# Kernel optimization log

Hardware: AMD Instinct MI355X
Metric: run time of the kernel (lower is better)

Reference implementation:

```python
import jax, jax.numpy as jnp
import numpy as np

N_NODES = 100000
M_EDGES = 500000
D = 128
L = 2
LRELU_SLOPE = 0.01
LN_EPS = 1e-5


def layer_norm(x, g, b):
    mu = jnp.mean(x, axis=-1, keepdims=True)
    var = jnp.var(x, axis=-1, keepdims=True)
    return (x - mu) * jax.lax.rsqrt(var + LN_EPS) * g + b


def leaky_relu(x):
    return jnp.where(x >= 0, x, LRELU_SLOPE * x)


def setup_inputs() -> dict:
    key = jax.random.key(0)
    ks = jax.random.split(key, 12)
    s = 1.0 / np.sqrt(D)
    inp = {
        "H": jax.random.normal(ks[0], (N_NODES, D), jnp.float32),
        "E": jax.random.normal(ks[1], (M_EDGES, D), jnp.float32),
        "ht": jax.random.randint(ks[2], (M_EDGES, 2), 0, N_NODES, jnp.int64) if jax.config.jax_enable_x64 else jax.random.randint(ks[2], (M_EDGES, 2), 0, N_NODES).astype(jnp.int32),
        "queries": jax.random.randint(ks[3], (M_EDGES,), 0, 2).astype(jnp.int32),
        # per-layer params stacked on leading L axis
        "W_eu": jax.random.uniform(ks[4], (L, 3 * D, D), jnp.float32, -s, s),
        "b_eu": jnp.zeros((L, D), jnp.float32),
        "ln_e_g": jnp.ones((L, D), jnp.float32),
        "ln_e_b": jnp.zeros((L, D), jnp.float32),
        "W_fwd": jax.random.uniform(ks[5], (L, 2 * D, D), jnp.float32, -s, s),
        "b_fwd": jnp.zeros((L, D), jnp.float32),
        "W_back": jax.random.uniform(ks[6], (L, 2 * D, D), jnp.float32, -s, s),
        "b_back": jnp.zeros((L, D), jnp.float32),
        "ln_h_g": jnp.ones((L, D), jnp.float32),
        "ln_h_b": jnp.zeros((L, D), jnp.float32),
    }
    return inp


def aggregate_messages(ht, messages_fwd, messages_back, n):
    # destinations: fwd msgs go to tails, back msgs go to heads
    msg_dst = jnp.concatenate([ht[:, 1], ht[:, 0]])  # [2m]
    messages = jnp.concatenate([messages_fwd, messages_back], axis=0)  # [2m, d]
    agg = jax.ops.segment_sum(messages, msg_dst, num_segments=n)  # [n, d]
    counts = jax.ops.segment_sum(jnp.ones_like(msg_dst, jnp.float32), msg_dst, num_segments=n)
    # torch yields nan/inf for count-0 nodes; clamp to 1 (0/1 = 0) for stability
    return agg / jnp.maximum(counts, 1.0)[:, None]


def reference(H, E, ht, queries, W_eu, b_eu, ln_e_g, ln_e_b,
              W_fwd, b_fwd, W_back, b_back, ln_h_g, ln_h_b):
    n = H.shape[0]
    for l in range(L):
        # --- EdgeUpdateLayer ---
        head_rep = H[ht[:, 0]]  # [m, d]
        tail_rep = H[ht[:, 1]]  # [m, d]
        triple = jnp.concatenate([head_rep, E, tail_rep], axis=1)  # [m, 3d]
        eu = leaky_relu(triple @ W_eu[l] + b_eu[l])
        E = layer_norm(eu + E, ln_e_g[l], ln_e_b[l])
        # --- MessagePassingLayer ---
        msgs_fwd = jnp.concatenate([H[ht[:, 0]], E], axis=1) @ W_fwd[l] + b_fwd[l]
        msgs_back = jnp.concatenate([H[ht[:, 1]], E], axis=1) @ W_back[l] + b_back[l]
        agg = aggregate_messages(ht, msgs_fwd, msgs_back, n)
        H = layer_norm(leaky_relu(agg) + H, ln_h_g[l], ln_h_b[l])
    return H
```

## Files before the change

kernel.cpp:

```cpp
#include <hip/hip_runtime.h>

#define N_NODES 100000
#define M_EDGES 500000
#define D 128
#define SLOPE 0.01f
#define EPS 1e-5f

typedef __attribute__((ext_vector_type(8))) short bf16x8;
typedef __attribute__((ext_vector_type(4))) float f32x4;
typedef __attribute__((ext_vector_type(4))) unsigned int u32x4;

__device__ __forceinline__ unsigned short f2bf(float f) {
    union { float f; unsigned u; } v; v.f = f;
    unsigned r = v.u + 0x7FFF + ((v.u >> 16) & 1);
    return (unsigned short)(r >> 16);
}
__device__ __forceinline__ float bf2f(unsigned short u) {
    union { unsigned u; float f; } v; v.u = ((unsigned)u) << 16; return v.f;
}
__device__ __forceinline__ u32x4 pack8v(f32x4 a, f32x4 b) {
    u32x4 r;
    r.x = ((unsigned)f2bf(a.y) << 16) | f2bf(a.x);
    r.y = ((unsigned)f2bf(a.w) << 16) | f2bf(a.z);
    r.z = ((unsigned)f2bf(b.y) << 16) | f2bf(b.x);
    r.w = ((unsigned)f2bf(b.w) << 16) | f2bf(b.z);
    return r;
}

__global__ void wconv_kernel(const float* __restrict__ src, unsigned short* __restrict__ dst,
                             int K, int total)
{
    int i = blockIdx.x * 256 + threadIdx.x;
    if (i >= total) return;
    int layer_sz = K * 128;
    int l = i / layer_sz;
    int r = i - l * layer_sz;
    int j    = r & 7;
    int lane = (r >> 3) & 63;
    int nt   = (r >> 9) & 7;
    int kk   = r >> 12;
    int row  = kk * 32 + ((lane >> 4) << 3) + j;
    int col  = nt * 16 + (lane & 15);
    dst[i] = f2bf(src[(size_t)l * layer_sz + row * 128 + col]);
}

__global__ void h2b_kernel(const float* __restrict__ src, unsigned short* __restrict__ dst, int total8)
{
    int i = blockIdx.x * 256 + threadIdx.x;
    if (i >= total8) return;
    f32x4 a = ((const f32x4*)src)[2 * i];
    f32x4 b = ((const f32x4*)src)[2 * i + 1];
    ((u32x4*)dst)[i] = pack8v(a, b);
}

__global__ void count_kernel(const int* __restrict__ ht, int* __restrict__ cnt, int m)
{
    int e = blockIdx.x * 256 + threadIdx.x;
    if (e < m) {
        atomicAdd(&cnt[ht[2 * e]],     1);
        atomicAdd(&cnt[ht[2 * e + 1]], 1);
    }
}

__global__ void scanA_kernel(const int* __restrict__ cnt, int* __restrict__ partial,
                             int* __restrict__ bsum, int n)
{
    __shared__ int tmp[256];
    int t = threadIdx.x, i = blockIdx.x * 256 + t;
    int v = (i < n) ? cnt[i] : 0;
    tmp[t] = v;
    __syncthreads();
    for (int s = 1; s < 256; s <<= 1) {
        int x = (t >= s) ? tmp[t - s] : 0;
        __syncthreads();
        tmp[t] += x;
        __syncthreads();
    }
    if (i < n) partial[i] = tmp[t] - v;
    if (t == 255) bsum[blockIdx.x] = tmp[255];
}

__global__ void scanB_kernel(int* __restrict__ bsum, int nb)
{
    __shared__ int tmp[512];
    int t = threadIdx.x;
    int v = (t < nb) ? bsum[t] : 0;
    tmp[t] = v;
    __syncthreads();
    for (int s = 1; s < 512; s <<= 1) {
        int x = (t >= s) ? tmp[t - s] : 0;
        __syncthreads();
        tmp[t] += x;
        __syncthreads();
    }
    if (t < nb) bsum[t] = tmp[t] - v;
}

__global__ void scanC_kernel(const int* __restrict__ partial, const int* __restrict__ bsum,
                             int* __restrict__ off, int* __restrict__ pos, int n)
{
    int i = blockIdx.x * 256 + threadIdx.x;
    if (i < n) {
        int o = partial[i] + bsum[blockIdx.x];
        off[i] = o;
        pos[i] = o;
    }
    if (i == 0) off[n] = 2 * M_EDGES;
}

__global__ void fill_kernel(const int* __restrict__ ht, int* __restrict__ pos,
                            int* __restrict__ slotF, int* __restrict__ slotB, int m)
{
    int e = blockIdx.x * 256 + threadIdx.x;
    if (e < m) {
        int2 p = ((const int2*)ht)[e];
        slotF[e] = atomicAdd(&pos[p.y], 1);
        slotB[e] = atomicAdd(&pos[p.x], 1);
    }
}

template <bool E_F32, bool WRITE_E>
__global__ __launch_bounds__(64, 2)
void edge_mfma_kernel(const unsigned short* __restrict__ Hb,
                      const float* __restrict__ E0,
                      const unsigned short* __restrict__ Ebf,
                      unsigned short* __restrict__ Eout,
                      const int* __restrict__ ht,
                      const unsigned short* __restrict__ Weu,
                      const unsigned short* __restrict__ Wf,
                      const unsigned short* __restrict__ Wb,
                      const float* __restrict__ beu,
                      const float* __restrict__ lneg, const float* __restrict__ lneb,
                      const float* __restrict__ bfw, const float* __restrict__ bbw,
                      const int* __restrict__ slotF, const int* __restrict__ slotB,
                      unsigned short* __restrict__ msg)
{
    __shared__ unsigned char en[16384];

    const int ln  = threadIdx.x;
    const int g   = ln >> 4;
    const int c15 = ln & 15;
    const int ew0 = blockIdx.x * 64;

    int eL = ew0 + ln; if (eL >= M_EDGES) eL = M_EDGES - 1;
    const int slotFv = slotF[eL];
    const int slotBv = slotB[eL];

#pragma unroll
    for (int it = 0; it < 16; ++it) {
        int lin = it * 1024 + ln * 16;
        int row = lin >> 8;
        int e   = ew0 + row;
        int es  = (e < M_EDGES) ? e : (M_EDGES - 1);
        int elem = (lin & 255) >> 1;
        u32x4 pk;
        if (E_F32) {
            const float* s = E0 + (size_t)es * D + elem;
            pk = pack8v(*(const f32x4*)s, *(const f32x4*)(s + 4));
        } else {
            pk = *(const u32x4*)(Ebf + (size_t)es * D + elem);
        }
        *(u32x4*)(en + (lin ^ ((row & 7) << 4))) = pk;
    }

    const unsigned short* hrow[4];
    const unsigned short* trow[4];
#pragma unroll
    for (int m = 0; m < 4; ++m) {
        int e = ew0 + m * 16 + c15;
        int es = (e < M_EDGES) ? e : (M_EDGES - 1);
        int2 p = ((const int2*)ht)[es];
        hrow[m] = Hb + (size_t)p.x * D;
        trow[m] = Hb + (size_t)p.y * D;
    }
    const int swz = (c15 & 7) << 4;

    f32x4 acc[4][8];

#pragma unroll
    for (int m = 0; m < 4; ++m)
#pragma unroll
        for (int nt = 0; nt < 8; ++nt) acc[m][nt] = (f32x4){0.f, 0.f, 0.f, 0.f};

    {
        const u32x4* Wg = (const u32x4*)Weu;
        u32x4 bc[8];
        bf16x8 a[4], an[4];
        auto loadA = [&](int kk, int m) -> bf16x8 {
            if (kk < 4)
                return *(const bf16x8*)(hrow[m] + kk * 32 + g * 8);
            if (kk < 8)
                return *(const bf16x8*)(en + (((m * 16 + c15) * 256 + (kk - 4) * 64 + g * 16) ^ swz));
            return *(const bf16x8*)(trow[m] + (kk - 8) * 32 + g * 8);
        };
#pragma unroll
        for (int nt = 0; nt < 8; ++nt) bc[nt] = Wg[nt * 64 + ln];
#pragma unroll
        for (int m = 0; m < 4; ++m) a[m] = loadA(0, m);
#pragma unroll
        for (int kk = 0; kk < 12; ++kk) {
            if (kk < 11) {
#pragma unroll
                for (int m = 0; m < 4; ++m) an[m] = loadA(kk + 1, m);
            }
#pragma unroll
            for (int nt = 0; nt < 8; ++nt) {
                bf16x8 b = *(const bf16x8*)&bc[nt];
#pragma unroll
                for (int m = 0; m < 4; ++m)
                    acc[m][nt] = __builtin_amdgcn_mfma_f32_16x16x32_bf16(a[m], b, acc[m][nt], 0, 0, 0);
                if (kk < 11) bc[nt] = Wg[(kk + 1) * 512 + nt * 64 + ln];
            }
#pragma unroll
            for (int m = 0; m < 4; ++m) a[m] = an[m];
        }
    }

    {
        float be[8], lg[8], lb[8];
#pragma unroll
        for (int nt = 0; nt < 8; ++nt) {
            be[nt] = beu[nt * 16 + c15];
            lg[nt] = lneg[nt * 16 + c15];
            lb[nt] = lneb[nt * 16 + c15];
        }
#pragma unroll
        for (int m = 0; m < 4; ++m) {
            float s[4] = {0.f,0.f,0.f,0.f}, ss[4] = {0.f,0.f,0.f,0.f};
#pragma unroll
            for (int nt = 0; nt < 8; ++nt) {
#pragma unroll
                for (int r = 0; r < 4; ++r) {
                    int row = m * 16 + g * 4 + r;
                    float x = acc[m][nt][r] + be[nt];
                    x = (x >= 0.f) ? x : SLOPE * x;
                    int lin = row * 256 + (nt * 16 + c15) * 2;
                    x += bf2f(*(const unsigned short*)(en + (lin ^ ((row & 7) << 4))));
                    acc[m][nt][r] = x;
                    s[r] += x; ss[r] += x * x;
                }
            }
#pragma unroll
            for (int d = 1; d < 16; d <<= 1) {
#pragma unroll
                for (int r = 0; r < 4; ++r) {
                    s[r]  += __shfl_xor(s[r],  d);
                    ss[r] += __shfl_xor(ss[r], d);
                }
            }
            float mu[4], rs[4];
#pragma unroll
            for (int r = 0; r < 4; ++r) {
                mu[r] = s[r] * (1.0f / 128.0f);
                float var = ss[r] * (1.0f / 128.0f) - mu[r] * mu[r];
                rs[r] = rsqrtf(var + EPS);
            }
#pragma unroll
            for (int nt = 0; nt < 8; ++nt) {
#pragma unroll
                for (int r = 0; r < 4; ++r) {
                    int row = m * 16 + g * 4 + r;
                    float xn = (acc[m][nt][r] - mu[r]) * rs[r] * lg[nt] + lb[nt];
                    int lin = row * 256 + (nt * 16 + c15) * 2;
                    *(unsigned short*)(en + (lin ^ ((row & 7) << 4))) = f2bf(xn);
                }
            }
        }
    }

    if (WRITE_E) {
#pragma unroll
        for (int it = 0; it < 16; ++it) {
            int lin = it * 1024 + ln * 16;
            int row = lin >> 8;
            int e   = ew0 + row;
            if (e < M_EDGES)
                *(u32x4*)(Eout + (size_t)e * D + ((lin & 255) >> 1)) =
                    *(const u32x4*)(en + (lin ^ ((row & 7) << 4)));
        }
    }

#pragma unroll
    for (int pass = 0; pass < 2; ++pass) {
        const u32x4* Wg = (const u32x4*)(pass == 0 ? Wf : Wb);
#pragma unroll
        for (int m = 0; m < 4; ++m)
#pragma unroll
            for (int nt = 0; nt < 8; ++nt) acc[m][nt] = (f32x4){0.f, 0.f, 0.f, 0.f};

        {
            u32x4 bc[8];
            bf16x8 a[4], an[4];
            auto loadA = [&](int kk, int m) -> bf16x8 {
                if (kk < 4)
                    return *(const bf16x8*)((pass == 0 ? hrow[m] : trow[m]) + kk * 32 + g * 8);
                return *(const bf16x8*)(en + (((m * 16 + c15) * 256 + (kk - 4) * 64 + g * 16) ^ swz));
            };
#pragma unroll
            for (int nt = 0; nt < 8; ++nt) bc[nt] = Wg[nt * 64 + ln];
#pragma unroll
            for (int m = 0; m < 4; ++m) a[m] = loadA(0, m);
#pragma unroll
            for (int kk = 0; kk < 8; ++kk) {
                if (kk < 7) {
#pragma unroll
                    for (int m = 0; m < 4; ++m) an[m] = loadA(kk + 1, m);
                }
#pragma unroll
                for (int nt = 0; nt < 8; ++nt) {
                    bf16x8 b = *(const bf16x8*)&bc[nt];
#pragma unroll
                    for (int m = 0; m < 4; ++m)
                        acc[m][nt] = __builtin_amdgcn_mfma_f32_16x16x32_bf16(a[m], b, acc[m][nt], 0, 0, 0);
                    if (kk < 7) bc[nt] = Wg[(kk + 1) * 512 + nt * 64 + ln];
                }
#pragma unroll
                for (int m = 0; m < 4; ++m) a[m] = an[m];
            }
        }

        {
            const float* bias = pass == 0 ? bfw : bbw;
            const int slotv = pass == 0 ? slotFv : slotBv;
            float bv[8];
#pragma unroll
            for (int nt = 0; nt < 8; ++nt) bv[nt] = bias[nt * 16 + c15];
#pragma unroll
            for (int m = 0; m < 4; ++m) {
#pragma unroll
                for (int r = 0; r < 4; ++r) {
                    int erow = m * 16 + g * 4 + r;
                    bool val = (ew0 + erow < M_EDGES);
                    int slot = __shfl(slotv, erow);
                    unsigned* base = (unsigned*)(msg + (size_t)slot * D + (c15 & ~1));
#pragma unroll
                    for (int nt = 0; nt < 8; ++nt) {
                        float v = acc[m][nt][r] + bv[nt];
                        float o = __shfl_xor(v, 1);
                        float lo = (ln & 1) ? o : v;
                        float hi = (ln & 1) ? v : o;
                        unsigned pk = ((unsigned)f2bf(hi) << 16) | f2bf(lo);
                        if (val && ((ln & 1) == (nt >> 2)))
                            base[nt * 8] = pk;
                    }
                }
            }
        }
    }
}

__global__ __launch_bounds__(256)
void node_kernel(const float* __restrict__ Hin, const unsigned short* __restrict__ msg,
                 const int* __restrict__ off, const float* __restrict__ g,
                 const float* __restrict__ b, float* __restrict__ Hout,
                 unsigned short* __restrict__ Hb, int n)
{
    const int wave = threadIdx.x >> 6, lane = threadIdx.x & 63;
    const int node = blockIdx.x * 4 + wave;
    if (node >= n) return;

    const int beg = off[node], end = off[node + 1];
    const float inv = 1.0f / fmaxf((float)(end - beg), 1.0f);
    const unsigned* mb = (const unsigned*)msg;

    float a0 = 0.f, a1 = 0.f;
    int i = beg;
    for (; i + 1 < end; i += 2) {
        unsigned v0 = mb[(size_t)i * 64 + lane];
        unsigned v1 = mb[(size_t)(i + 1) * 64 + lane];
        a0 += bf2f((unsigned short)(v0 & 0xffff)) + bf2f((unsigned short)(v1 & 0xffff));
        a1 += bf2f((unsigned short)(v0 >> 16))    + bf2f((unsigned short)(v1 >> 16));
    }
    if (i < end) {
        unsigned v0 = mb[(size_t)i * 64 + lane];
        a0 += bf2f((unsigned short)(v0 & 0xffff));
        a1 += bf2f((unsigned short)(v0 >> 16));
    }

    a0 *= inv; a1 *= inv;
    a0 = (a0 >= 0.f) ? a0 : SLOPE * a0;
    a1 = (a1 >= 0.f) ? a1 : SLOPE * a1;

    size_t base = (size_t)node * D + 2 * lane;
    float x0 = a0 + Hin[base];
    float x1 = a1 + Hin[base + 1];

    float s = x0 + x1, ss = x0 * x0 + x1 * x1;
#pragma unroll
    for (int d = 1; d < 64; d <<= 1) {
        s  += __shfl_xor(s, d);
        ss += __shfl_xor(ss, d);
    }
    float mu  = s * (1.0f / 128.0f);
    float var = ss * (1.0f / 128.0f) - mu * mu;
    float rs  = rsqrtf(var + EPS);

    float o0 = (x0 - mu) * rs * g[2 * lane]     + b[2 * lane];
    float o1 = (x1 - mu) * rs * g[2 * lane + 1] + b[2 * lane + 1];
    Hout[base]     = o0;
    Hout[base + 1] = o1;
    Hb[base]       = f2bf(o0);
    Hb[base + 1]   = f2bf(o1);
}

extern "C" void kernel_launch(void* const* d_in, const int* in_sizes, int n_in,
                              void* d_out, int out_size, void* d_ws, size_t ws_size,
                              hipStream_t stream)
{
    const float* H0   = (const float*)d_in[0];
    const float* E0   = (const float*)d_in[1];
    const int*   ht   = (const int*)d_in[2];
    const float* Weu  = (const float*)d_in[4];
    const float* beu  = (const float*)d_in[5];
    const float* lneg = (const float*)d_in[6];
    const float* lneb = (const float*)d_in[7];
    const float* Wf   = (const float*)d_in[8];
    const float* bfw  = (const float*)d_in[9];
    const float* Wb   = (const float*)d_in[10];
    const float* bbw  = (const float*)d_in[11];
    const float* lnhg = (const float*)d_in[12];
    const float* lnhb = (const float*)d_in[13];

    float* Hout = (float*)d_out;

    char* ws = (char*)d_ws;
    unsigned short* msg    = (unsigned short*)(ws);
    unsigned short* Ebuf   = (unsigned short*)(ws + 256000000);
    unsigned short* Hb     = (unsigned short*)(ws + 384000000);
    unsigned short* Weu_sw = (unsigned short*)(ws + 409600000);
    unsigned short* Wf_sw  = (unsigned short*)(ws + 409796608);
    unsigned short* Wb_sw  = (unsigned short*)(ws + 409927680);
    int*            cnt    = (int*)(ws + 410058752);
    int*            partial= (int*)(ws + 410458752);
    int*            bsum   = (int*)(ws + 410858752);
    int*            off    = (int*)(ws + 410860800);
    int*            pos    = (int*)(ws + 411260816);
    int*            slotF  = (int*)(ws + 411660816);
    int*            slotB  = (int*)(ws + 413660816);

    wconv_kernel<<<(2*384*128 + 255)/256, 256, 0, stream>>>(Weu, Weu_sw, 384, 2*384*128);
    wconv_kernel<<<(2*256*128 + 255)/256, 256, 0, stream>>>(Wf,  Wf_sw,  256, 2*256*128);
    wconv_kernel<<<(2*256*128 + 255)/256, 256, 0, stream>>>(Wb,  Wb_sw,  256, 2*256*128);
    h2b_kernel<<<(N_NODES * D / 8 + 255)/256, 256, 0, stream>>>(H0, Hb, N_NODES * D / 8);

    const int nscan = (N_NODES + 255) / 256;
    hipMemsetAsync(cnt, 0, (size_t)N_NODES * sizeof(int), stream);
    count_kernel<<<(M_EDGES + 255) / 256, 256, 0, stream>>>(ht, cnt, M_EDGES);
    scanA_kernel<<<nscan, 256, 0, stream>>>(cnt, partial, bsum, N_NODES);
    scanB_kernel<<<1, 512, 0, stream>>>(bsum, nscan);
    scanC_kernel<<<nscan, 256, 0, stream>>>(partial, bsum, off, pos, N_NODES);
    fill_kernel<<<(M_EDGES + 255) / 256, 256, 0, stream>>>(ht, pos, slotF, slotB, M_EDGES);

    const int eblocks = (M_EDGES + 63) / 64;

    for (int l = 0; l < 2; ++l) {
        const float* Hin = (l == 0) ? H0 : Hout;

        if (l == 0) {
            edge_mfma_kernel<true, true><<<eblocks, 64, 0, stream>>>(
                Hb, E0, nullptr, Ebuf, ht,
                Weu_sw, Wf_sw, Wb_sw,
                beu, lneg, lneb, bfw, bbw, slotF, slotB, msg);
        } else {
            edge_mfma_kernel<false, false><<<eblocks, 64, 0, stream>>>(
                Hb, nullptr, Ebuf, nullptr, ht,
                Weu_sw + 49152, Wf_sw + 32768, Wb_sw + 32768,
                beu + D, lneg + D, lneb + D, bfw + D, bbw + D, slotF, slotB, msg);
        }

        node_kernel<<<(N_NODES + 3) / 4, 256, 0, stream>>>(
            Hin, msg, off, lnhg + (size_t)l * D, lnhb + (size_t)l * D, Hout, Hb, N_NODES);
    }
}
```

Baseline: 1.017 ms.

## Split edge kernel output columns across two waves per 64-edge block

```diff
diff --git a/kernel.cpp b/kernel.cpp
--- a/kernel.cpp
+++ b/kernel.cpp
@@ -120,7 +120,7 @@
 }
 
 template <bool E_F32, bool WRITE_E>
-__global__ __launch_bounds__(64, 2)
+__global__ __launch_bounds__(128, 3)
 void edge_mfma_kernel(const unsigned short* __restrict__ Hb,
                       const float* __restrict__ E0,
                       const unsigned short* __restrict__ Ebf,
@@ -136,19 +136,23 @@
                       unsigned short* __restrict__ msg)
 {
     __shared__ unsigned char en[16384];
-
-    const int ln  = threadIdx.x;
+    __shared__ float2 part[2][64];
+
+    const int tid = threadIdx.x;
+    const int wv  = tid >> 6;
+    const int ln  = tid & 63;
     const int g   = ln >> 4;
     const int c15 = ln & 15;
     const int ew0 = blockIdx.x * 64;
+    const int ntb = wv * 4;
 
     int eL = ew0 + ln; if (eL >= M_EDGES) eL = M_EDGES - 1;
     const int slotFv = slotF[eL];
     const int slotBv = slotB[eL];
 
 #pragma unroll
-    for (int it = 0; it < 16; ++it) {
-        int lin = it * 1024 + ln * 16;
+    for (int it = 0; it < 8; ++it) {
+        int lin = it * 2048 + tid * 16;
         int row = lin >> 8;
         int e   = ew0 + row;
         int es  = (e < M_EDGES) ? e : (M_EDGES - 1);
@@ -175,16 +179,18 @@
     }
     const int swz = (c15 & 7) << 4;
 
-    f32x4 acc[4][8];
+    __syncthreads();
+
+    f32x4 acc[4][4];
 
 #pragma unroll
     for (int m = 0; m < 4; ++m)
 #pragma unroll
-        for (int nt = 0; nt < 8; ++nt) acc[m][nt] = (f32x4){0.f, 0.f, 0.f, 0.f};
+        for (int nt = 0; nt < 4; ++nt) acc[m][nt] = (f32x4){0.f, 0.f, 0.f, 0.f};
 
     {
         const u32x4* Wg = (const u32x4*)Weu;
-        u32x4 bc[8];
+        u32x4 bc[4];
         bf16x8 a[4], an[4];
         auto loadA = [&](int kk, int m) -> bf16x8 {
             if (kk < 4)
@@ -194,7 +200,7 @@
             return *(const bf16x8*)(trow[m] + (kk - 8) * 32 + g * 8);
         };
 #pragma unroll
-        for (int nt = 0; nt < 8; ++nt) bc[nt] = Wg[nt * 64 + ln];
+        for (int nt = 0; nt < 4; ++nt) bc[nt] = Wg[(ntb + nt) * 64 + ln];
 #pragma unroll
         for (int m = 0; m < 4; ++m) a[m] = loadA(0, m);
 #pragma unroll
@@ -204,12 +210,12 @@
                 for (int m = 0; m < 4; ++m) an[m] = loadA(kk + 1, m);
             }
 #pragma unroll
-            for (int nt = 0; nt < 8; ++nt) {
+            for (int nt = 0; nt < 4; ++nt) {
                 bf16x8 b = *(const bf16x8*)&bc[nt];
 #pragma unroll
                 for (int m = 0; m < 4; ++m)
                     acc[m][nt] = __builtin_amdgcn_mfma_f32_16x16x32_bf16(a[m], b, acc[m][nt], 0, 0, 0);
-                if (kk < 11) bc[nt] = Wg[(kk + 1) * 512 + nt * 64 + ln];
+                if (kk < 11) bc[nt] = Wg[(kk + 1) * 512 + (ntb + nt) * 64 + ln];
             }
 #pragma unroll
             for (int m = 0; m < 4; ++m) a[m] = an[m];
@@ -217,24 +223,25 @@
     }
 
     {
-        float be[8], lg[8], lb[8];
-#pragma unroll
-        for (int nt = 0; nt < 8; ++nt) {
-            be[nt] = beu[nt * 16 + c15];
-            lg[nt] = lneg[nt * 16 + c15];
-            lb[nt] = lneb[nt * 16 + c15];
+        float be[4], lg4[4], lb4[4];
+#pragma unroll
+        for (int nt = 0; nt < 4; ++nt) {
+            int idx = (ntb + nt) * 16 + c15;
+            be[nt]  = beu[idx];
+            lg4[nt] = lneg[idx];
+            lb4[nt] = lneb[idx];
         }
 #pragma unroll
         for (int m = 0; m < 4; ++m) {
             float s[4] = {0.f,0.f,0.f,0.f}, ss[4] = {0.f,0.f,0.f,0.f};
 #pragma unroll
-            for (int nt = 0; nt < 8; ++nt) {
+            for (int nt = 0; nt < 4; ++nt) {
 #pragma unroll
                 for (int r = 0; r < 4; ++r) {
                     int row = m * 16 + g * 4 + r;
                     float x = acc[m][nt][r] + be[nt];
                     x = (x >= 0.f) ? x : SLOPE * x;
-                    int lin = row * 256 + (nt * 16 + c15) * 2;
+                    int lin = row * 256 + ((ntb + nt) * 16 + c15) * 2;
                     x += bf2f(*(const unsigned short*)(en + (lin ^ ((row & 7) << 4))));
                     acc[m][nt][r] = x;
                     s[r] += x; ss[r] += x * x;
@@ -248,35 +255,53 @@
                     ss[r] += __shfl_xor(ss[r], d);
                 }
             }
+            if (c15 == 0) {
+#pragma unroll
+                for (int r = 0; r < 4; ++r)
+                    part[wv][m * 16 + g * 4 + r] = make_float2(s[r], ss[r]);
+            }
+        }
+        __syncthreads();
+#pragma unroll
+        for (int m = 0; m < 4; ++m) {
             float mu[4], rs[4];
 #pragma unroll
             for (int r = 0; r < 4; ++r) {
-                mu[r] = s[r] * (1.0f / 128.0f);
-                float var = ss[r] * (1.0f / 128.0f) - mu[r] * mu[r];
+                int row = m * 16 + g * 4 + r;
+                float2 po = part[wv ^ 1][row];
+                float2 ps = part[wv][row];
+                float sm  = ps.x + po.x;
+                float sq  = ps.y + po.y;
+                mu[r] = sm * (1.0f / 128.0f);
+                float var = sq * (1.0f / 128.0f) - mu[r] * mu[r];
                 rs[r] = rsqrtf(var + EPS);
             }
 #pragma unroll
-            for (int nt = 0; nt < 8; ++nt) {
+            for (int nt = 0; nt < 4; ++nt) {
 #pragma unroll
                 for (int r = 0; r < 4; ++r) {
                     int row = m * 16 + g * 4 + r;
-                    float xn = (acc[m][nt][r] - mu[r]) * rs[r] * lg[nt] + lb[nt];
-                    int lin = row * 256 + (nt * 16 + c15) * 2;
+                    float xn = (acc[m][nt][r] - mu[r]) * rs[r] * lg4[nt] + lb4[nt];
+                    int lin = row * 256 + ((ntb + nt) * 16 + c15) * 2;
                     *(unsigned short*)(en + (lin ^ ((row & 7) << 4))) = f2bf(xn);
                 }
             }
         }
     }
+    __syncthreads();
 
     if (WRITE_E) {
 #pragma unroll
-        for (int it = 0; it < 16; ++it) {
-            int lin = it * 1024 + ln * 16;
-            int row = lin >> 8;
+        for (int it = 0; it < 8; ++it) {
+            int idx = it * 64 + ln;
+            int row = idx >> 3;
+            int sub = idx & 7;
             int e   = ew0 + row;
-            if (e < M_EDGES)
-                *(u32x4*)(Eout + (size_t)e * D + ((lin & 255) >> 1)) =
+            if (e < M_EDGES) {
+                int lin = row * 256 + wv * 128 + sub * 16;
+                *(u32x4*)(Eout + (size_t)e * D + wv * 64 + sub * 8) =
                     *(const u32x4*)(en + (lin ^ ((row & 7) << 4)));
+            }
         }
     }
 
@@ -286,10 +311,10 @@
 #pragma unroll
         for (int m = 0; m < 4; ++m)
 #pragma unroll
-            for (int nt = 0; nt < 8; ++nt) acc[m][nt] = (f32x4){0.f, 0.f, 0.f, 0.f};
+            for (int nt = 0; nt < 4; ++nt) acc[m][nt] = (f32x4){0.f, 0.f, 0.f, 0.f};
 
         {
-            u32x4 bc[8];
+            u32x4 bc[4];
             bf16x8 a[4], an[4];
             auto loadA = [&](int kk, int m) -> bf16x8 {
                 if (kk < 4)
@@ -297,7 +322,7 @@
                 return *(const bf16x8*)(en + (((m * 16 + c15) * 256 + (kk - 4) * 64 + g * 16) ^ swz));
             };
 #pragma unroll
-            for (int nt = 0; nt < 8; ++nt) bc[nt] = Wg[nt * 64 + ln];
+            for (int nt = 0; nt < 4; ++nt) bc[nt] = Wg[(ntb + nt) * 64 + ln];
 #pragma unroll
             for (int m = 0; m < 4; ++m) a[m] = loadA(0, m);
 #pragma unroll
@@ -307,12 +332,12 @@
                     for (int m = 0; m < 4; ++m) an[m] = loadA(kk + 1, m);
                 }
 #pragma unroll
-                for (int nt = 0; nt < 8; ++nt) {
+                for (int nt = 0; nt < 4; ++nt) {
                     bf16x8 b = *(const bf16x8*)&bc[nt];
 #pragma unroll
                     for (int m = 0; m < 4; ++m)
                         acc[m][nt] = __builtin_amdgcn_mfma_f32_16x16x32_bf16(a[m], b, acc[m][nt], 0, 0, 0);
-                    if (kk < 7) bc[nt] = Wg[(kk + 1) * 512 + nt * 64 + ln];
+                    if (kk < 7) bc[nt] = Wg[(kk + 1) * 512 + (ntb + nt) * 64 + ln];
                 }
 #pragma unroll
                 for (int m = 0; m < 4; ++m) a[m] = an[m];
@@ -322,9 +347,9 @@
         {
             const float* bias = pass == 0 ? bfw : bbw;
             const int slotv = pass == 0 ? slotFv : slotBv;
-            float bv[8];
-#pragma unroll
-            for (int nt = 0; nt < 8; ++nt) bv[nt] = bias[nt * 16 + c15];
+            float bv[4];
+#pragma unroll
+            for (int nt = 0; nt < 4; ++nt) bv[nt] = bias[(ntb + nt) * 16 + c15];
 #pragma unroll
             for (int m = 0; m < 4; ++m) {
 #pragma unroll
@@ -332,15 +357,15 @@
                     int erow = m * 16 + g * 4 + r;
                     bool val = (ew0 + erow < M_EDGES);
                     int slot = __shfl(slotv, erow);
-                    unsigned* base = (unsigned*)(msg + (size_t)slot * D + (c15 & ~1));
-#pragma unroll
-                    for (int nt = 0; nt < 8; ++nt) {
+                    unsigned* base = (unsigned*)(msg + (size_t)slot * D + wv * 64 + (c15 & ~1));
+#pragma unroll
+                    for (int nt = 0; nt < 4; ++nt) {
                         float v = acc[m][nt][r] + bv[nt];
                         float o = __shfl_xor(v, 1);
                         float lo = (ln & 1) ? o : v;
                         float hi = (ln & 1) ? v : o;
                         unsigned pk = ((unsigned)f2bf(hi) << 16) | f2bf(lo);
-                        if (val && ((ln & 1) == (nt >> 2)))
+                        if (val && ((ln & 1) == (nt >> 1)))
                             base[nt * 8] = pk;
                     }
                 }
@@ -457,12 +482,12 @@
         const float* Hin = (l == 0) ? H0 : Hout;
 
         if (l == 0) {
-            edge_mfma_kernel<true, true><<<eblocks, 64, 0, stream>>>(
+            edge_mfma_kernel<true, true><<<eblocks, 128, 0, stream>>>(
                 Hb, E0, nullptr, Ebuf, ht,
                 Weu_sw, Wf_sw, Wb_sw,
                 beu, lneg, lneb, bfw, bbw, slotF, slotB, msg);
         } else {
-            edge_mfma_kernel<false, false><<<eblocks, 64, 0, stream>>>(
+            edge_mfma_kernel<false, false><<<eblocks, 128, 0, stream>>>(
                 Hb, nullptr, Ebuf, nullptr, ht,
                 Weu_sw + 49152, Wf_sw + 32768, Wb_sw + 32768,
                 beu + D, lneg + D, lneb + D, bfw + D, bbw + D, slotF, slotB, msg);
```

Measured after the change: 1.565 ms. 1.54x slower.

## Precompute per-node H@W products and gather them instead of edge-level matmuls

Applied to the files above, without the earlier changes.

```diff
diff --git a/kernel.cpp b/kernel.cpp
--- a/kernel.cpp
+++ b/kernel.cpp
@@ -26,6 +26,7 @@
     r.w = ((unsigned)f2bf(b.w) << 16) | f2bf(b.z);
     return r;
 }
+#define GXT(v, nt) bf2f((unsigned short)(((nt) & 1) ? ((v)[(nt) >> 1] >> 16) : ((v)[(nt) >> 1] & 0xffff)))
 
 __global__ void wconv_kernel(const float* __restrict__ src, unsigned short* __restrict__ dst,
                              int K, int total)
@@ -119,9 +120,83 @@
     }
 }
 
+__global__ __launch_bounds__(256, 2)
+void hw_kernel(const unsigned short* __restrict__ Hb,
+               const unsigned short* __restrict__ B0,
+               const unsigned short* __restrict__ B1,
+               const unsigned short* __restrict__ B2,
+               const unsigned short* __restrict__ B3,
+               unsigned short* __restrict__ HW)
+{
+    __shared__ unsigned short bsh[16384];
+
+    const int tid = threadIdx.x;
+    const int wv  = tid >> 6;
+    const int ln  = tid & 63;
+    const int g   = ln >> 4;
+    const int c15 = ln & 15;
+    const int mb  = blockIdx.x >> 2;
+    const int grp = blockIdx.x & 3;
+
+    const unsigned short* Bsel = (grp == 0) ? B0 : (grp == 1) ? B1 : (grp == 2) ? B2 : B3;
+
+    {
+        const u32x4* bs = (const u32x4*)Bsel;
+        u32x4* bd = (u32x4*)bsh;
+#pragma unroll
+        for (int it = 0; it < 8; ++it) bd[it * 256 + tid] = bs[it * 256 + tid];
+    }
+
+    const int rb = mb * 128 + wv * 32;
+    const unsigned short* arow[2];
+#pragma unroll
+    for (int m = 0; m < 2; ++m) {
+        int r = rb + m * 16 + c15;
+        if (r >= N_NODES) r = N_NODES - 1;
+        arow[m] = Hb + (size_t)r * 128;
+    }
+    __syncthreads();
+
+    f32x4 acc[2][8];
+#pragma unroll
+    for (int m = 0; m < 2; ++m)
+#pragma unroll
+        for (int nt = 0; nt < 8; ++nt) acc[m][nt] = (f32x4){0.f, 0.f, 0.f, 0.f};
+
+#pragma unroll
+    for (int kk = 0; kk < 4; ++kk) {
+        bf16x8 a[2];
+#pragma unroll
+        for (int m = 0; m < 2; ++m) a[m] = *(const bf16x8*)(arow[m] + kk * 32 + g * 8);
+#pragma unroll
+        for (int nt = 0; nt < 8; ++nt) {
+            bf16x8 b = *(const bf16x8*)(bsh + (kk * 8 + nt) * 512 + ln * 8);
+#pragma unroll
+            for (int m = 0; m < 2; ++m)
+                acc[m][nt] = __builtin_amdgcn_mfma_f32_16x16x32_bf16(a[m], b, acc[m][nt], 0, 0, 0);
+        }
+    }
+
+#pragma unroll
+    for (int m = 0; m < 2; ++m) {
+#pragma unroll
+        for (int rr = 0; rr < 4; ++rr) {
+            int rg = rb + m * 16 + g * 4 + rr;
+            if (rg < N_NODES) {
+                u32x4 o;
+                o.x = ((unsigned)f2bf(acc[m][1][rr]) << 16) | f2bf(acc[m][0][rr]);
+                o.y = ((unsigned)f2bf(acc[m][3][rr]) << 16) | f2bf(acc[m][2][rr]);
+                o.z = ((unsigned)f2bf(acc[m][5][rr]) << 16) | f2bf(acc[m][4][rr]);
+                o.w = ((unsigned)f2bf(acc[m][7][rr]) << 16) | f2bf(acc[m][6][rr]);
+                *(u32x4*)(HW + (size_t)rg * 512 + grp * 128 + c15 * 8) = o;
+            }
+        }
+    }
+}
+
 template <bool E_F32, bool WRITE_E>
 __global__ __launch_bounds__(64, 2)
-void edge_mfma_kernel(const unsigned short* __restrict__ Hb,
+void edge_mfma_kernel(const unsigned short* __restrict__ HW,
                       const float* __restrict__ E0,
                       const unsigned short* __restrict__ Ebf,
                       unsigned short* __restrict__ Eout,
@@ -135,84 +210,83 @@
                       const int* __restrict__ slotF, const int* __restrict__ slotB,
                       unsigned short* __restrict__ msg)
 {
-    __shared__ unsigned char en[16384];
+    __shared__ unsigned char en[8192];
 
     const int ln  = threadIdx.x;
     const int g   = ln >> 4;
     const int c15 = ln & 15;
-    const int ew0 = blockIdx.x * 64;
-
-    int eL = ew0 + ln; if (eL >= M_EDGES) eL = M_EDGES - 1;
-    const int slotFv = slotF[eL];
-    const int slotBv = slotB[eL];
-
-#pragma unroll
-    for (int it = 0; it < 16; ++it) {
+    const int ew0 = blockIdx.x * 32;
+
+    const int slotFv = slotF[ew0 + (ln & 31)];
+    const int slotBv = slotB[ew0 + (ln & 31)];
+
+    int hid[2][4], tln[2][4];
+#pragma unroll
+    for (int m = 0; m < 2; ++m)
+#pragma unroll
+        for (int rr = 0; rr < 4; ++rr) {
+            int2 p = ((const int2*)ht)[ew0 + m * 16 + g * 4 + rr];
+            hid[m][rr] = p.x;
+            tln[m][rr] = p.y;
+        }
+
+    u32x4 ga[2][4], gc[2][4];
+#pragma unroll
+    for (int m = 0; m < 2; ++m)
+#pragma unroll
+        for (int rr = 0; rr < 4; ++rr) {
+            ga[m][rr] = *(const u32x4*)(HW + (size_t)hid[m][rr] * 512 + c15 * 8);
+            gc[m][rr] = *(const u32x4*)(HW + (size_t)tln[m][rr] * 512 + 128 + c15 * 8);
+        }
+
+#pragma unroll
+    for (int it = 0; it < 8; ++it) {
         int lin = it * 1024 + ln * 16;
         int row = lin >> 8;
         int e   = ew0 + row;
-        int es  = (e < M_EDGES) ? e : (M_EDGES - 1);
         int elem = (lin & 255) >> 1;
         u32x4 pk;
         if (E_F32) {
-            const float* s = E0 + (size_t)es * D + elem;
+            const float* s = E0 + (size_t)e * D + elem;
             pk = pack8v(*(const f32x4*)s, *(const f32x4*)(s + 4));
         } else {
-            pk = *(const u32x4*)(Ebf + (size_t)es * D + elem);
+            pk = *(const u32x4*)(Ebf + (size_t)e * D + elem);
         }
         *(u32x4*)(en + (lin ^ ((row & 7) << 4))) = pk;
     }
 
-    const unsigned short* hrow[4];
-    const unsigned short* trow[4];
-#pragma unroll
-    for (int m = 0; m < 4; ++m) {
-        int e = ew0 + m * 16 + c15;
-        int es = (e < M_EDGES) ? e : (M_EDGES - 1);
-        int2 p = ((const int2*)ht)[es];
-        hrow[m] = Hb + (size_t)p.x * D;
-        trow[m] = Hb + (size_t)p.y * D;
-    }
-    const int swz = (c15 & 7) << 4;
-
-    f32x4 acc[4][8];
-
-#pragma unroll
-    for (int m = 0; m < 4; ++m)
+    const int ebase0 = c15 * 256 + g * 16;
+    const int ebase1 = (16 + c15) * 256 + g * 16;
+    const int swz    = (c15 & 7) << 4;
+
+    f32x4 acc[2][8];
+
+#pragma unroll
+    for (int m = 0; m < 2; ++m)
 #pragma unroll
         for (int nt = 0; nt < 8; ++nt) acc[m][nt] = (f32x4){0.f, 0.f, 0.f, 0.f};
-
     {
         const u32x4* Wg = (const u32x4*)Weu;
         u32x4 bc[8];
-        bf16x8 a[4], an[4];
-        auto loadA = [&](int kk, int m) -> bf16x8 {
-            if (kk < 4)
-                return *(const bf16x8*)(hrow[m] + kk * 32 + g * 8);
-            if (kk < 8)
-                return *(const bf16x8*)(en + (((m * 16 + c15) * 256 + (kk - 4) * 64 + g * 16) ^ swz));
-            return *(const bf16x8*)(trow[m] + (kk - 8) * 32 + g * 8);
-        };
-#pragma unroll
-        for (int nt = 0; nt < 8; ++nt) bc[nt] = Wg[nt * 64 + ln];
-#pragma unroll
-        for (int m = 0; m < 4; ++m) a[m] = loadA(0, m);
-#pragma unroll
-        for (int kk = 0; kk < 12; ++kk) {
-            if (kk < 11) {
-#pragma unroll
-                for (int m = 0; m < 4; ++m) an[m] = loadA(kk + 1, m);
+        bf16x8 a0, a1, a0n, a1n;
+#pragma unroll
+        for (int nt = 0; nt < 8; ++nt) bc[nt] = Wg[4 * 512 + nt * 64 + ln];
+        a0 = *(const bf16x8*)(en + (ebase0 ^ swz));
+        a1 = *(const bf16x8*)(en + (ebase1 ^ swz));
+#pragma unroll
+        for (int kk = 0; kk < 4; ++kk) {
+            if (kk < 3) {
+                a0n = *(const bf16x8*)(en + ((ebase0 + (kk + 1) * 64) ^ swz));
+                a1n = *(const bf16x8*)(en + ((ebase1 + (kk + 1) * 64) ^ swz));
             }
 #pragma unroll
             for (int nt = 0; nt < 8; ++nt) {
                 bf16x8 b = *(const bf16x8*)&bc[nt];
-#pragma unroll
-                for (int m = 0; m < 4; ++m)
-                    acc[m][nt] = __builtin_amdgcn_mfma_f32_16x16x32_bf16(a[m], b, acc[m][nt], 0, 0, 0);
-                if (kk < 11) bc[nt] = Wg[(kk + 1) * 512 + nt * 64 + ln];
-            }
-#pragma unroll
-            for (int m = 0; m < 4; ++m) a[m] = an[m];
+                acc[0][nt] = __builtin_amdgcn_mfma_f32_16x16x32_bf16(a0, b, acc[0][nt], 0, 0, 0);
+                acc[1][nt] = __builtin_amdgcn_mfma_f32_16x16x32_bf16(a1, b, acc[1][nt], 0, 0, 0);
+                if (kk < 3) bc[nt] = Wg[(5 + kk) * 512 + nt * 64 + ln];
+            }
+            a0 = a0n; a1 = a1n;
         }
     }
 
@@ -225,14 +299,14 @@
             lb[nt] = lneb[nt * 16 + c15];
         }
 #pragma unroll
-        for (int m = 0; m < 4; ++m) {
+        for (int m = 0; m < 2; ++m) {
             float s[4] = {0.f,0.f,0.f,0.f}, ss[4] = {0.f,0.f,0.f,0.f};
 #pragma unroll
             for (int nt = 0; nt < 8; ++nt) {
 #pragma unroll
                 for (int r = 0; r < 4; ++r) {
                     int row = m * 16 + g * 4 + r;
-                    float x = acc[m][nt][r] + be[nt];
+                    float x = acc[m][nt][r] + GXT(ga[m][r], nt) + GXT(gc[m][r], nt) + be[nt];
                     x = (x >= 0.f) ? x : SLOPE * x;
                     int lin = row * 256 + (nt * 16 + c15) * 2;
                     x += bf2f(*(const unsigned short*)(en + (lin ^ ((row & 7) << 4))));
@@ -270,77 +344,76 @@
 
     if (WRITE_E) {
 #pragma unroll
-        for (int it = 0; it < 16; ++it) {
+        for (int it = 0; it < 8; ++it) {
             int lin = it * 1024 + ln * 16;
             int row = lin >> 8;
-            int e   = ew0 + row;
-            if (e < M_EDGES)
-                *(u32x4*)(Eout + (size_t)e * D + ((lin & 255) >> 1)) =
-                    *(const u32x4*)(en + (lin ^ ((row & 7) << 4)));
-        }
-    }
-
-#pragma unroll
-    for (int pass = 0; pass < 2; ++pass) {
-        const u32x4* Wg = (const u32x4*)(pass == 0 ? Wf : Wb);
-#pragma unroll
-        for (int m = 0; m < 4; ++m)
+            *(u32x4*)(Eout + (size_t)(ew0 + row) * D + ((lin & 255) >> 1)) =
+                *(const u32x4*)(en + (lin ^ ((row & 7) << 4)));
+        }
+    }
+
+#pragma unroll 1
+    for (int p = 0; p < 2; ++p) {
+        const u32x4* Wg = (const u32x4*)(p ? Wb : Wf);
+        const float* bias = p ? bbw : bfw;
+        const int slotv = p ? slotBv : slotFv;
+
+        u32x4 gm[2][4];
+#pragma unroll
+        for (int m = 0; m < 2; ++m)
+#pragma unroll
+            for (int rr = 0; rr < 4; ++rr) {
+                int node = p ? tln[m][rr] : hid[m][rr];
+                gm[m][rr] = *(const u32x4*)(HW + (size_t)node * 512 + 256 + p * 128 + c15 * 8);
+            }
+
+#pragma unroll
+        for (int m = 0; m < 2; ++m)
 #pragma unroll
             for (int nt = 0; nt < 8; ++nt) acc[m][nt] = (f32x4){0.f, 0.f, 0.f, 0.f};
-
         {
             u32x4 bc[8];
-            bf16x8 a[4], an[4];
-            auto loadA = [&](int kk, int m) -> bf16x8 {
-                if (kk < 4)
-                    return *(const bf16x8*)((pass == 0 ? hrow[m] : trow[m]) + kk * 32 + g * 8);
-                return *(const bf16x8*)(en + (((m * 16 + c15) * 256 + (kk - 4) * 64 + g * 16) ^ swz));
-            };
-#pragma unroll
-            for (int nt = 0; nt < 8; ++nt) bc[nt] = Wg[nt * 64 + ln];
-#pragma unroll
-            for (int m = 0; m < 4; ++m) a[m] = loadA(0, m);
-#pragma unroll
-            for (int kk = 0; kk < 8; ++kk) {
-                if (kk < 7) {
-#pragma unroll
-                    for (int m = 0; m < 4; ++m) an[m] = loadA(kk + 1, m);
+            bf16x8 a0, a1, a0n, a1n;
+#pragma unroll
+            for (int nt = 0; nt < 8; ++nt) bc[nt] = Wg[4 * 512 + nt * 64 + ln];
+            a0 = *(const bf16x8*)(en + (ebase0 ^ swz));
+            a1 = *(const bf16x8*)(en + (ebase1 ^ swz));
+#pragma unroll
+            for (int kk = 0; kk < 4; ++kk) {
+                if (kk < 3) {
+                    a0n = *(const bf16x8*)(en + ((ebase0 + (kk + 1) * 64) ^ swz));
+                    a1n = *(const bf16x8*)(en + ((ebase1 + (kk + 1) * 64) ^ swz));
                 }
 #pragma unroll
                 for (int nt = 0; nt < 8; ++nt) {
                     bf16x8 b = *(const bf16x8*)&bc[nt];
-#pragma unroll
-                    for (int m = 0; m < 4; ++m)
-                        acc[m][nt] = __builtin_amdgcn_mfma_f32_16x16x32_bf16(a[m], b, acc[m][nt], 0, 0, 0);
-                    if (kk < 7) bc[nt] = Wg[(kk + 1) * 512 + nt * 64 + ln];
+                    acc[0][nt] = __builtin_amdgcn_mfma_f32_16x16x32_bf16(a0, b, acc[0][nt], 0, 0, 0);
+                    acc[1][nt] = __builtin_amdgcn_mfma_f32_16x16x32_bf16(a1, b, acc[1][nt], 0, 0, 0);
+                    if (kk < 3) bc[nt] = Wg[(5 + kk) * 512 + nt * 64 + ln];
                 }
-#pragma unroll
-                for (int m = 0; m < 4; ++m) a[m] = an[m];
+                a0 = a0n; a1 = a1n;
             }
         }
 
         {
-            const float* bias = pass == 0 ? bfw : bbw;
-            const int slotv = pass == 0 ? slotFv : slotBv;
             float bv[8];
 #pragma unroll
             for (int nt = 0; nt < 8; ++nt) bv[nt] = bias[nt * 16 + c15];
 #pragma unroll
-            for (int m = 0; m < 4; ++m) {
+            for (int m = 0; m < 2; ++m) {
 #pragma unroll
                 for (int r = 0; r < 4; ++r) {
                     int erow = m * 16 + g * 4 + r;
-                    bool val = (ew0 + erow < M_EDGES);
                     int slot = __shfl(slotv, erow);
                     unsigned* base = (unsigned*)(msg + (size_t)slot * D + (c15 & ~1));
 #pragma unroll
                     for (int nt = 0; nt < 8; ++nt) {
-                        float v = acc[m][nt][r] + bv[nt];
+                        float v = acc[m][nt][r] + GXT(gm[m][r], nt) + bv[nt];
                         float o = __shfl_xor(v, 1);
                         float lo = (ln & 1) ? o : v;
                         float hi = (ln & 1) ? v : o;
                         unsigned pk = ((unsigned)f2bf(hi) << 16) | f2bf(lo);
-                        if (val && ((ln & 1) == (nt >> 2)))
+                        if ((ln & 1) == (nt >> 2))
                             base[nt * 8] = pk;
                     }
                 }
@@ -426,17 +499,18 @@
     char* ws = (char*)d_ws;
     unsigned short* msg    = (unsigned short*)(ws);
     unsigned short* Ebuf   = (unsigned short*)(ws + 256000000);
-    unsigned short* Hb     = (unsigned short*)(ws + 384000000);
-    unsigned short* Weu_sw = (unsigned short*)(ws + 409600000);
-    unsigned short* Wf_sw  = (unsigned short*)(ws + 409796608);
-    unsigned short* Wb_sw  = (unsigned short*)(ws + 409927680);
-    int*            cnt    = (int*)(ws + 410058752);
-    int*            partial= (int*)(ws + 410458752);
-    int*            bsum   = (int*)(ws + 410858752);
-    int*            off    = (int*)(ws + 410860800);
-    int*            pos    = (int*)(ws + 411260816);
-    int*            slotF  = (int*)(ws + 411660816);
-    int*            slotB  = (int*)(ws + 413660816);
+    unsigned short* HW     = (unsigned short*)(ws + 384000000);
+    unsigned short* Hb     = (unsigned short*)(ws + 486400000);
+    unsigned short* Weu_sw = (unsigned short*)(ws + 512000000);
+    unsigned short* Wf_sw  = (unsigned short*)(ws + 512196608);
+    unsigned short* Wb_sw  = (unsigned short*)(ws + 512327680);
+    int*            cnt    = (int*)(ws + 512458752);
+    int*            partial= (int*)(ws + 512858752);
+    int*            bsum   = (int*)(ws + 513258752);
+    int*            off    = (int*)(ws + 513260800);
+    int*            pos    = (int*)(ws + 513660816);
+    int*            slotF  = (int*)(ws + 514060816);
+    int*            slotB  = (int*)(ws + 516060816);
 
     wconv_kernel<<<(2*384*128 + 255)/256, 256, 0, stream>>>(Weu, Weu_sw, 384, 2*384*128);
     wconv_kernel<<<(2*256*128 + 255)/256, 256, 0, stream>>>(Wf,  Wf_sw,  256, 2*256*128);
@@ -451,20 +525,25 @@
     scanC_kernel<<<nscan, 256, 0, stream>>>(partial, bsum, off, pos, N_NODES);
     fill_kernel<<<(M_EDGES + 255) / 256, 256, 0, stream>>>(ht, pos, slotF, slotB, M_EDGES);
 
-    const int eblocks = (M_EDGES + 63) / 64;
+    const int hwblocks = ((N_NODES + 127) / 128) * 4;
+    const int eblocks  = M_EDGES / 32;
 
     for (int l = 0; l < 2; ++l) {
         const float* Hin = (l == 0) ? H0 : Hout;
+        const unsigned short* WeuL = Weu_sw + (size_t)l * 49152;
+        const unsigned short* WfL  = Wf_sw  + (size_t)l * 32768;
+        const unsigned short* WbL  = Wb_sw  + (size_t)l * 32768;
+
+        hw_kernel<<<hwblocks, 256, 0, stream>>>(
+            Hb, WeuL, WeuL + 8 * 4096, WfL, WbL, HW);
 
         if (l == 0) {
             edge_mfma_kernel<true, true><<<eblocks, 64, 0, stream>>>(
-                Hb, E0, nullptr, Ebuf, ht,
-                Weu_sw, Wf_sw, Wb_sw,
+                HW, E0, nullptr, Ebuf, ht, WeuL, WfL, WbL,
                 beu, lneg, lneb, bfw, bbw, slotF, slotB, msg);
         } else {
             edge_mfma_kernel<false, false><<<eblocks, 64, 0, stream>>>(
-                Hb, nullptr, Ebuf, nullptr, ht,
-                Weu_sw + 49152, Wf_sw + 32768, Wb_sw + 32768,
+                HW, nullptr, Ebuf, nullptr, ht, WeuL, WfL, WbL,
                 beu + D, lneg + D, lneb + D, bfw + D, bbw + D, slotF, slotB, msg);
         }
 
```

Measured after the change: 863.1 us. -15.2%, faster.
